# Kernel tuning notes

Measured on AMD Instinct MI355X. Metric: run time of the kernel, lower is better.

The kernel has to match this reference:

```python
import jax, jax.numpy as jnp
import numpy as np

D_MODEL = 1024
N_HEADS = 16
D_K = 64
CHUNK_LEN = 64
B, CHUNKS, NEIGHBORS, NEIGHBOR_LEN = 8, 32, 2, 128
SEQ = CHUNKS * CHUNK_LEN  # 2048
LN_EPS = 1e-5


def setup_inputs() -> dict:
    key = jax.random.key(0)
    ks = jax.random.split(key, 8)
    s = 0.02
    return {
        "h": jax.random.normal(ks[0], (B, SEQ, D_MODEL), dtype=jnp.float32),
        "e": jax.random.normal(ks[1], (B, CHUNKS, NEIGHBORS, NEIGHBOR_LEN, D_MODEL), dtype=jnp.float32),
        "Wq": jax.random.normal(ks[2], (D_MODEL, N_HEADS * D_K), dtype=jnp.float32) * s,
        "bq": jnp.zeros((N_HEADS * D_K,), dtype=jnp.float32),
        "Wk": jax.random.normal(ks[3], (D_MODEL, N_HEADS * D_K), dtype=jnp.float32) * s,
        "bk": jnp.zeros((N_HEADS * D_K,), dtype=jnp.float32),
        "Wv": jax.random.normal(ks[4], (D_MODEL, N_HEADS * D_K), dtype=jnp.float32) * s,
        "bv": jnp.zeros((N_HEADS * D_K,), dtype=jnp.float32),
        "gamma": jnp.ones((D_MODEL,), dtype=jnp.float32),
        "beta": jnp.zeros((D_MODEL,), dtype=jnp.float32),
        "Wo": jax.random.normal(ks[5], (N_HEADS * D_K, D_MODEL), dtype=jnp.float32) * s,
        "bo": jnp.zeros((D_MODEL,), dtype=jnp.float32),
    }


def _layer_norm(x, gamma, beta):
    mu = jnp.mean(x, axis=-1, keepdims=True)
    var = jnp.mean(jnp.square(x - mu), axis=-1, keepdims=True)
    return (x - mu) * jax.lax.rsqrt(var + LN_EPS) * gamma + beta


def reference(h, e, Wq, bq, Wk, bk, Wv, bv, gamma, beta, Wo, bo):
    batch, chunks, neighbors, neighbor_len, d_model = e.shape
    seq = h.shape[1]
    scale = 1.0 / np.sqrt(D_K)
    h_res = h

    # shift so each chunk attends only to completed retrieval chunks
    x = h[:, CHUNK_LEN - 1:]                      # [b, seq-(cl-1), d]
    x = _layer_norm(x, gamma, beta)
    pad = chunks * CHUNK_LEN - x.shape[1]
    x = jnp.pad(x, ((0, 0), (0, pad), (0, 0)))    # [b, chunks*cl, d]
    x = x.reshape(batch, chunks, CHUNK_LEN, d_model)

    q = (x @ Wq + bq).reshape(batch, chunks, CHUNK_LEN, N_HEADS, D_K)
    k = (e @ Wk + bk).reshape(batch, chunks, neighbors, neighbor_len, N_HEADS, D_K)
    v = (e @ Wv + bv).reshape(batch, chunks, neighbors, neighbor_len, N_HEADS, D_K)

    attn = jnp.einsum('bcihd,bcnjhd->bchinj', q, k) * scale   # [b,c,h,i,n,j]
    a_shape = attn.shape
    attn = jax.nn.softmax(attn.reshape(*a_shape[:4], -1), axis=-1).reshape(a_shape)

    o = jnp.einsum('bchinj,bcnjhd->bcihd', attn, v)           # [b,c,i,h,d]
    o = o.reshape(batch, chunks * CHUNK_LEN, N_HEADS * D_K)
    o = o @ Wo + bo
    # undo the shift: left-pad by chunk_len-1, truncate to seq
    o = jnp.pad(o, ((0, 0), (CHUNK_LEN - 1, 0), (0, 0)))[:, :seq]
    return o + h_res
```

## Files before the change

kernel.cpp:

```cpp
#include <hip/hip_runtime.h>
#include <hip/hip_bf16.h>

typedef __attribute__((ext_vector_type(8))) short bf16x8;
typedef __attribute__((ext_vector_type(4))) float f32x4;
typedef __attribute__((ext_vector_type(8))) unsigned short u16x8;

static __device__ __forceinline__ unsigned short f2bf(float f) {
  unsigned int u = __builtin_bit_cast(unsigned int, f);
  u += 0x7fffu + ((u >> 16) & 1u);
  return (unsigned short)(u >> 16);
}
static __device__ __forceinline__ unsigned int pk2(float lo, float hi) {
  return (unsigned int)f2bf(lo) | ((unsigned int)f2bf(hi) << 16);
}
static __device__ __forceinline__ void gload_lds16(const void* g, void* l) {
  __builtin_amdgcn_global_load_lds(
      (__attribute__((address_space(1))) void*)(g),
      (__attribute__((address_space(3))) void*)(l), 16, 0, 0);
}

__global__ __launch_bounds__(256) void cvt_bf16(const float* __restrict__ in,
                                                unsigned short* __restrict__ out,
                                                long n8) {
  const long stride = (long)gridDim.x * 256;
  for (long i = (long)blockIdx.x * 256 + threadIdx.x; i < n8; i += stride) {
    const float4 a = ((const float4*)in)[2 * i];
    const float4 b = ((const float4*)in)[2 * i + 1];
    uint4 w;
    w.x = pk2(a.x, a.y);
    w.y = pk2(a.z, a.w);
    w.z = pk2(b.x, b.y);
    w.w = pk2(b.z, b.w);
    ((uint4*)out)[i] = w;
  }
}

__global__ __launch_bounds__(256) void transpose_w(const float* __restrict__ W,
                                                   unsigned short* __restrict__ WT) {
  __shared__ float tile[64][65];
  const int bx = blockIdx.x;
  const int by = blockIdx.y;
  const int t = threadIdx.x;
  const int rr = t >> 6;
  const int cc = t & 63;
#pragma unroll
  for (int i = 0; i < 16; ++i) {
    int r = i * 4 + rr;
    tile[r][cc] = W[(size_t)(by * 64 + r) * 1024 + bx * 64 + cc];
  }
  __syncthreads();
#pragma unroll
  for (int i = 0; i < 16; ++i) {
    int n = i * 4 + rr;
    WT[(size_t)(bx * 64 + n) * 1024 + by * 64 + cc] = f2bf(tile[cc][n]);
  }
}

__global__ __launch_bounds__(256) void ln_kernel(const float* __restrict__ H,
                                                 const float* __restrict__ gamma,
                                                 const float* __restrict__ beta,
                                                 unsigned short* __restrict__ X) {
  const int row = blockIdx.x;
  const int b = row >> 11;
  const int t = row & 2047;
  const int tid = threadIdx.x;
  uint2* xo = (uint2*)(X + (size_t)row * 1024);
  if (t >= 1985) {
    uint2 z;
    z.x = 0;
    z.y = 0;
    xo[tid] = z;
    return;
  }
  const float4* hp = (const float4*)(H + (size_t)(b * 2048 + t + 63) * 1024);
  float4 v = hp[tid];
  float s = v.x + v.y + v.z + v.w;
  float q = v.x * v.x + v.y * v.y + v.z * v.z + v.w * v.w;
#pragma unroll
  for (int off = 32; off > 0; off >>= 1) {
    s += __shfl_down(s, off);
    q += __shfl_down(q, off);
  }
  __shared__ float red[8];
  const int lane = tid & 63, wid = tid >> 6;
  if (lane == 0) {
    red[wid] = s;
    red[4 + wid] = q;
  }
  __syncthreads();
  s = red[0] + red[1] + red[2] + red[3];
  q = red[4] + red[5] + red[6] + red[7];
  const float mu = s * (1.0f / 1024.0f);
  const float var = q * (1.0f / 1024.0f) - mu * mu;
  const float rs = rsqrtf(var + 1e-5f);
  const float4 g = ((const float4*)gamma)[tid];
  const float4 bb = ((const float4*)beta)[tid];
  uint2 w;
  w.x = pk2((v.x - mu) * rs * g.x + bb.x, (v.y - mu) * rs * g.y + bb.y);
  w.y = pk2((v.z - mu) * rs * g.z + bb.z, (v.w - mu) * rs * g.w + bb.w);
  xo[tid] = w;
}

__global__ __launch_bounds__(256) void fill_head(const float* __restrict__ H,
                                                 float* __restrict__ OUT) {
  const int idx = blockIdx.x * 256 + threadIdx.x;
  const int b = idx / 16128;
  const int rem = idx - b * 16128;
  const size_t off = (size_t)b * 524288 + rem;
  ((float4*)OUT)[off] = ((const float4*)H)[off];
}

#define FENCE_BAR()                                  \
  {                                                  \
    asm volatile("" ::: "memory");                   \
    __builtin_amdgcn_s_barrier();                    \
    __builtin_amdgcn_sched_barrier(0);               \
  }
#define VMW2() asm volatile("s_waitcnt vmcnt(2)" ::: "memory")

#define LDA_(mh, buf)                                                                   \
  {                                                                                     \
    const char* base_ = (const char*)&lds[buf][wm][0];                                  \
    _Pragma("unroll") for (int mi = 0; mi < 4; ++mi) {                                  \
      const int r_ = (mh) * 64 + mi * 16 + lrow;                                        \
      af[mi][0] = *(const bf16x8*)(base_ + r_ * 128 + (((0 + lk) ^ (r_ & 7)) * 16));    \
      af[mi][1] = *(const bf16x8*)(base_ + r_ * 128 + (((4 + lk) ^ (r_ & 7)) * 16));    \
    }                                                                                   \
  }
#define LDB_(nh, buf)                                                                   \
  {                                                                                     \
    const char* base_ = (const char*)&lds[buf][2 + (wn >> 1)][0];                       \
    _Pragma("unroll") for (int ni = 0; ni < 2; ++ni) {                                  \
      const int r_ = (wn & 1) * 64 + (nh) * 32 + ni * 16 + lrow;                        \
      bfr[nh][ni][0] =                                                                  \
          *(const bf16x8*)(base_ + r_ * 128 + (((0 + lk) ^ (r_ & 7)) * 16));            \
      bfr[nh][ni][1] =                                                                  \
          *(const bf16x8*)(base_ + r_ * 128 + (((4 + lk) ^ (r_ & 7)) * 16));            \
    }                                                                                   \
  }
#define MMA_(mh, nh)                                                                    \
  {                                                                                     \
    __builtin_amdgcn_s_setprio(1);                                                      \
    _Pragma("unroll") for (int mi = 0; mi < 4; ++mi)                                    \
        _Pragma("unroll") for (int ni = 0; ni < 2; ++ni) {                              \
      acc[(mh) * 4 + mi][(nh) * 2 + ni] = __builtin_amdgcn_mfma_f32_16x16x32_bf16(      \
          af[mi][0], bfr[nh][ni][0], acc[(mh) * 4 + mi][(nh) * 2 + ni], 0, 0, 0);       \
      acc[(mh) * 4 + mi][(nh) * 2 + ni] = __builtin_amdgcn_mfma_f32_16x16x32_bf16(      \
          af[mi][1], bfr[nh][ni][1], acc[(mh) * 4 + mi][(nh) * 2 + ni], 0, 0, 0);       \
    }                                                                                   \
    __builtin_amdgcn_s_setprio(0);                                                      \
  }

template <int MODE>
__global__ __launch_bounds__(512, 2) void gemm256(
    const unsigned short* __restrict__ A, const unsigned short* __restrict__ BT,
    const float* __restrict__ bias1, const float* __restrict__ bias2,
    unsigned short* __restrict__ C1, unsigned short* __restrict__ C2,
    const float* __restrict__ H, float* __restrict__ OUT) {
  __shared__ alignas(16) unsigned short lds[2][4][128 * 64];
  const int tid = threadIdx.x;
  const int lane = tid & 63;
  const int wid = tid >> 6;
  const int wm = wid >> 2, wn = wid & 3;
  const int lrow = lane & 15, lk = lane >> 4;

  const int nx = gridDim.x;
  const int orig = blockIdx.y * nx + blockIdx.x;
  const int cpx = (nx * gridDim.y) >> 3;
  const int swz = (orig & 7) * cpx + (orig >> 3);
  const int m0 = (swz / nx) * 256;
  const int n0 = (swz % nx) * 256;

  f32x4 acc[8][4] = {};
  bf16x8 af[4][2], bfr[2][2][2];

  auto STAGE = [&](int slot, int kt) {
    const int buf = kt & 1;
    const int kc = kt < 16 ? kt : 15;
    const unsigned short* src = (slot < 2) ? A + (size_t)(m0 + slot * 128) * 1024
                                           : BT + (size_t)(n0 + (slot - 2) * 128) * 1024;
    unsigned short* dst = &lds[buf][slot][0];
#pragma unroll
    for (int l = 0; l < 2; ++l) {
      const int row = l * 64 + wid * 8 + (lane >> 3);
      const int ch = (lane & 7) ^ (row & 7);
      gload_lds16(src + (size_t)row * 1024 + kc * 64 + ch * 8,
                  (char*)dst + (l * 64 + wid * 8) * 128);
    }
  };

  STAGE(0, 0);
  STAGE(1, 0);
  STAGE(2, 0);
  STAGE(3, 0);
  STAGE(0, 1);
  VMW2();
  __builtin_amdgcn_s_barrier();

  for (int it = 0; it < 8; ++it) {
    const int t = 2 * it;
    LDA_(0, 0);
    LDB_(0, 0);
    STAGE(1, t + 1);
    FENCE_BAR();
    MMA_(0, 0);
    FENCE_BAR();
    LDB_(1, 0);
    STAGE(2, t + 1);
    FENCE_BAR();
    MMA_(0, 1);
    FENCE_BAR();
    LDA_(1, 0);
    STAGE(3, t + 1);
    FENCE_BAR();
    MMA_(1, 1);
    FENCE_BAR();
    STAGE(0, t + 2);
    FENCE_BAR();
    MMA_(1, 0);
    VMW2();
    FENCE_BAR();
    LDA_(0, 1);
    LDB_(0, 1);
    STAGE(1, t + 2);
    FENCE_BAR();
    MMA_(0, 0);
    FENCE_BAR();
    LDB_(1, 1);
    STAGE(2, t + 2);
    FENCE_BAR();
    MMA_(0, 1);
    FENCE_BAR();
    LDA_(1, 1);
    STAGE(3, t + 2);
    FENCE_BAR();
    MMA_(1, 1);
    FENCE_BAR();
    STAGE(0, t + 3);
    FENCE_BAR();
    MMA_(1, 0);
    VMW2();
    FENCE_BAR();
  }

  if (MODE == 0) {
    const float* bsel = (n0 < 1024) ? bias1 : bias2;
    const int cbase = (n0 < 1024) ? n0 : (n0 - 1024);
    unsigned short* Cp0 = (n0 < 1024) ? C1 : C2;
    float bsv[4];
#pragma unroll
    for (int N = 0; N < 4; ++N) bsv[N] = bsel[cbase + wn * 64 + N * 16 + lrow];
    float* arr = (float*)&lds[0][0][0];
    const int q4 = lane >> 4;
    __syncthreads();
#pragma unroll
    for (int p = 0; p < 4; ++p) {
      if (wm == (p >> 1)) {
#pragma unroll
        for (int mb = 0; mb < 4; ++mb) {
          const int M = (p & 1) * 4 + mb;
#pragma unroll
          for (int N = 0; N < 4; ++N) {
            const int cl = wn * 64 + N * 16 + lrow;
#pragma unroll
            for (int r = 0; r < 4; ++r) {
              arr[(mb * 16 + q4 * 4 + r) * 260 + cl] = acc[M][N][r] + bsv[N];
            }
          }
        }
      }
      __syncthreads();
#pragma unroll
      for (int k = 0; k < 4; ++k) {
        const int chunk = k * 512 + tid;
        const int row = chunk >> 5;
        const int c8 = chunk & 31;
        const float* s = arr + row * 260 + c8 * 8;
        float4 f0 = *(const float4*)(s);
        float4 f1 = *(const float4*)(s + 4);
        uint4 w;
        w.x = pk2(f0.x, f0.y);
        w.y = pk2(f0.z, f0.w);
        w.z = pk2(f1.x, f1.y);
        w.w = pk2(f1.z, f1.w);
        *(uint4*)(Cp0 + (size_t)(m0 + p * 64 + row) * 1024 + cbase + c8 * 8) = w;
      }
      __syncthreads();
    }
  } else {
    const int r0 = lane >> 4;
#pragma unroll
    for (int N = 0; N < 4; ++N) {
      const int col = n0 + wn * 64 + N * 16 + lrow;
      const float bsv = bias1[col];
#pragma unroll
      for (int M = 0; M < 8; ++M) {
        const int row = m0 + wm * 128 + M * 16 + r0 * 4;
#pragma unroll
        for (int r = 0; r < 4; ++r) {
          const int gr = row + r;
          if ((gr & 2047) < 1985) {
            const size_t idx = (size_t)(gr + 63) * 1024 + col;
            OUT[idx] = H[idx] + acc[M][N][r] + bsv;
          }
        }
      }
    }
  }
}

__global__ __launch_bounds__(256) void attn_kernel(
    const unsigned short* __restrict__ Q, const unsigned short* __restrict__ K,
    const unsigned short* __restrict__ V, unsigned short* __restrict__ O) {
  __shared__ alignas(16) unsigned short k_lds[256 * 64];
  __shared__ alignas(16) unsigned short v_t[64 * 256];
  const int w = ((blockIdx.x & 7) << 9) | (blockIdx.x >> 3);
  const int h = w & 15;
  const int bc = w >> 4;
  const int tid = threadIdx.x;
  const int lane = tid & 63;
  const int wid = tid >> 6;
  const size_t kv0 = (size_t)bc * 256 * 1024 + h * 64;

  bf16x8 qf[2];
  {
    const size_t qrow = (size_t)bc * 64 + wid * 16 + (lane & 15);
    const unsigned short* qp = Q + qrow * 1024 + h * 64 + (lane >> 4) * 8;
    qf[0] = *(const bf16x8*)(qp);
    qf[1] = *(const bf16x8*)(qp + 32);
  }
#pragma unroll
  for (int it = 0; it < 8; ++it) {
    const int j = it * 32 + (tid >> 3);
    const int c = tid & 7;
    const uint4 kv = *(const uint4*)(K + kv0 + (size_t)j * 1024 + c * 8);
    *(uint4*)((char*)k_lds + j * 128 + ((c ^ (j & 7)) * 16)) = kv;
  }
  {
    const int j = (tid >> 1) * 2;
    const int half = tid & 1;
#pragma unroll
    for (int cc2 = 0; cc2 < 4; ++cc2) {
      const int chunk = half * 4 + cc2;
      const int d0 = chunk * 8;
      u16x8 a = *(const u16x8*)(V + kv0 + (size_t)j * 1024 + d0);
      u16x8 b = *(const u16x8*)(V + kv0 + (size_t)(j + 1) * 1024 + d0);
#pragma unroll
      for (int dd = 0; dd < 8; ++dd) {
        const int d = d0 + dd;
        unsigned int p = (unsigned int)a[dd] | ((unsigned int)b[dd] << 16);
        *(unsigned int*)((char*)v_t + d * 512 + (((j >> 3) ^ (d & 7)) * 16) + ((j & 7) * 2)) = p;
      }
    }
  }
  __syncthreads();

  f32x4 accs[16] = {};
#pragma unroll
  for (int jt = 0; jt < 16; ++jt) {
#pragma unroll
    for (int ks = 0; ks < 2; ++ks) {
      const int r = jt * 16 + (lane & 15);
      bf16x8 kf = *(const bf16x8*)((const char*)k_lds + r * 128 +
                                   (((ks * 4 + (lane >> 4)) ^ (r & 7)) * 16));
      accs[jt] = __builtin_amdgcn_mfma_f32_16x16x32_bf16(qf[ks], kf, accs[jt], 0, 0, 0);
    }
  }
  __syncthreads();

  float inv_[4];
#pragma unroll
  for (int r = 0; r < 4; ++r) {
    float m = accs[0][r];
#pragma unroll
    for (int jt = 1; jt < 16; ++jt) m = fmaxf(m, accs[jt][r]);
#pragma unroll
    for (int mk = 1; mk < 16; mk <<= 1) m = fmaxf(m, __shfl_xor(m, mk));
    float s = 0.f;
#pragma unroll
    for (int jt = 0; jt < 16; ++jt) {
      float p = __expf((accs[jt][r] - m) * 0.125f);
      accs[jt][r] = p;
      s += p;
    }
#pragma unroll
    for (int mk = 1; mk < 16; mk <<= 1) s += __shfl_xor(s, mk);
    inv_[r] = 1.0f / s;
  }
  char* pbase = (char*)k_lds + wid * 8192;
  {
    const int jc = lane & 15;
    const int i0 = (lane >> 4) * 4;
#pragma unroll
    for (int jt = 0; jt < 16; ++jt) {
      const int j = jt * 16 + jc;
#pragma unroll
      for (int r = 0; r < 4; ++r) {
        const int i = i0 + r;
        *(unsigned short*)(pbase + i * 512 + (((j >> 3) ^ (i & 7)) * 16) + ((j & 7) * 2)) =
            f2bf(accs[jt][r] * inv_[r]);
      }
    }
  }
  __syncthreads();

  f32x4 acco[4] = {};
#pragma unroll
  for (int jb = 0; jb < 8; ++jb) {
    const int i = lane & 15;
    bf16x8 pf = *(const bf16x8*)(pbase + i * 512 + (((jb * 4 + (lane >> 4)) ^ (i & 7)) * 16));
#pragma unroll
    for (int ni = 0; ni < 4; ++ni) {
      const int d = ni * 16 + (lane & 15);
      bf16x8 vf = *(const bf16x8*)((const char*)v_t + d * 512 +
                                   (((jb * 4 + (lane >> 4)) ^ (d & 7)) * 16));
      acco[ni] = __builtin_amdgcn_mfma_f32_16x16x32_bf16(pf, vf, acco[ni], 0, 0, 0);
    }
  }
  {
    const size_t row0 = (size_t)bc * 64 + wid * 16 + (lane >> 4) * 4;
#pragma unroll
    for (int ni = 0; ni < 4; ++ni) {
      const int col = h * 64 + ni * 16 + (lane & 15);
#pragma unroll
      for (int r = 0; r < 4; ++r) {
        O[(row0 + r) * 1024 + col] = f2bf(acco[ni][r]);
      }
    }
  }
}

extern "C" void kernel_launch(void* const* d_in, const int* in_sizes, int n_in,
                              void* d_out, int out_size, void* d_ws, size_t ws_size,
                              hipStream_t stream) {
  const float* h = (const float*)d_in[0];
  const float* e = (const float*)d_in[1];
  const float* Wq = (const float*)d_in[2];
  const float* bq = (const float*)d_in[3];
  const float* Wk = (const float*)d_in[4];
  const float* bk = (const float*)d_in[5];
  const float* Wv = (const float*)d_in[6];
  const float* bv = (const float*)d_in[7];
  const float* gamma = (const float*)d_in[8];
  const float* beta = (const float*)d_in[9];
  const float* Wo = (const float*)d_in[10];
  const float* bo = (const float*)d_in[11];
  float* out = (float*)d_out;

  char* ws = (char*)d_ws;
  unsigned short* x = (unsigned short*)ws;
  unsigned short* q = (unsigned short*)(ws + (32ull << 20));
  unsigned short* kbuf = (unsigned short*)(ws + (64ull << 20));
  unsigned short* vbuf = (unsigned short*)(ws + (192ull << 20));
  unsigned short* ebf = (unsigned short*)(ws + (320ull << 20));
  unsigned short* wqT = (unsigned short*)(ws + (448ull << 20));
  unsigned short* wkvT = (unsigned short*)(ws + (450ull << 20));
  unsigned short* woT = (unsigned short*)(ws + (454ull << 20));
  unsigned short* o = x;

  dim3 tb(256);
  cvt_bf16<<<2048, tb, 0, stream>>>(e, ebf, 8388608L);
  transpose_w<<<dim3(16, 16), tb, 0, stream>>>(Wq, wqT);
  transpose_w<<<dim3(16, 16), tb, 0, stream>>>(Wk, wkvT);
  transpose_w<<<dim3(16, 16), tb, 0, stream>>>(Wv, wkvT + 1024 * 1024);
  transpose_w<<<dim3(16, 16), tb, 0, stream>>>(Wo, woT);
  ln_kernel<<<16384, tb, 0, stream>>>(h, gamma, beta, x);
  gemm256<0><<<dim3(4, 64), dim3(512), 0, stream>>>(x, wqT, bq, nullptr, q, nullptr,
                                                    nullptr, nullptr);
  gemm256<0><<<dim3(8, 256), dim3(512), 0, stream>>>(ebf, wkvT, bk, bv, kbuf, vbuf,
                                                     nullptr, nullptr);
  attn_kernel<<<4096, tb, 0, stream>>>(q, kbuf, vbuf, o);
  fill_head<<<504, tb, 0, stream>>>(h, out);
  gemm256<1><<<dim3(4, 64), dim3(512), 0, stream>>>(o, woT, bo, nullptr, nullptr, nullptr,
                                                    h, out);
}
```

Measured before the change: 569.4 us.

## Double-buffer A fragments and cut barriers in the GEMM main loop

The 256x256 bf16 GEMM main loop gets separate register sets for the two A halves and two B halves. The second A and B fragments are now loaded while the first MMA block is still pending, and about half of the block-wide barriers are replaced by scheduling-only fences. This is meant to lower barrier stall time and overlap LDS reads with MFMA work. The cost is more VGPR pressure under the 512-thread, 2-block launch bound, plus reliance on the remaining barriers to keep LDS buffer reuse safe.

```diff
diff --git a/kernel.cpp b/kernel.cpp
--- a/kernel.cpp
+++ b/kernel.cpp
@@ -110,43 +110,42 @@
   ((float4*)OUT)[off] = ((const float4*)H)[off];
 }
 
-#define FENCE_BAR()                                  \
-  {                                                  \
-    asm volatile("" ::: "memory");                   \
-    __builtin_amdgcn_s_barrier();                    \
-    __builtin_amdgcn_sched_barrier(0);               \
-  }
+#define BAR()                                 \
+  {                                           \
+    asm volatile("" ::: "memory");            \
+    __builtin_amdgcn_s_barrier();             \
+    __builtin_amdgcn_sched_barrier(0);        \
+  }
+#define SB0() __builtin_amdgcn_sched_barrier(0)
 #define VMW2() asm volatile("s_waitcnt vmcnt(2)" ::: "memory")
 
-#define LDA_(mh, buf)                                                                   \
+#define LDA_(dst, mh, buf)                                                              \
   {                                                                                     \
     const char* base_ = (const char*)&lds[buf][wm][0];                                  \
     _Pragma("unroll") for (int mi = 0; mi < 4; ++mi) {                                  \
       const int r_ = (mh) * 64 + mi * 16 + lrow;                                        \
-      af[mi][0] = *(const bf16x8*)(base_ + r_ * 128 + (((0 + lk) ^ (r_ & 7)) * 16));    \
-      af[mi][1] = *(const bf16x8*)(base_ + r_ * 128 + (((4 + lk) ^ (r_ & 7)) * 16));    \
+      dst[mi][0] = *(const bf16x8*)(base_ + r_ * 128 + (((0 + lk) ^ (r_ & 7)) * 16));   \
+      dst[mi][1] = *(const bf16x8*)(base_ + r_ * 128 + (((4 + lk) ^ (r_ & 7)) * 16));   \
     }                                                                                   \
   }
-#define LDB_(nh, buf)                                                                   \
+#define LDB_(dst, nh, buf)                                                              \
   {                                                                                     \
     const char* base_ = (const char*)&lds[buf][2 + (wn >> 1)][0];                       \
     _Pragma("unroll") for (int ni = 0; ni < 2; ++ni) {                                  \
       const int r_ = (wn & 1) * 64 + (nh) * 32 + ni * 16 + lrow;                        \
-      bfr[nh][ni][0] =                                                                  \
-          *(const bf16x8*)(base_ + r_ * 128 + (((0 + lk) ^ (r_ & 7)) * 16));            \
-      bfr[nh][ni][1] =                                                                  \
-          *(const bf16x8*)(base_ + r_ * 128 + (((4 + lk) ^ (r_ & 7)) * 16));            \
+      dst[ni][0] = *(const bf16x8*)(base_ + r_ * 128 + (((0 + lk) ^ (r_ & 7)) * 16));   \
+      dst[ni][1] = *(const bf16x8*)(base_ + r_ * 128 + (((4 + lk) ^ (r_ & 7)) * 16));   \
     }                                                                                   \
   }
-#define MMA_(mh, nh)                                                                    \
+#define MMA_(mh, nh, A, B)                                                              \
   {                                                                                     \
     __builtin_amdgcn_s_setprio(1);                                                      \
     _Pragma("unroll") for (int mi = 0; mi < 4; ++mi)                                    \
         _Pragma("unroll") for (int ni = 0; ni < 2; ++ni) {                              \
       acc[(mh) * 4 + mi][(nh) * 2 + ni] = __builtin_amdgcn_mfma_f32_16x16x32_bf16(      \
-          af[mi][0], bfr[nh][ni][0], acc[(mh) * 4 + mi][(nh) * 2 + ni], 0, 0, 0);       \
+          A[mi][0], B[ni][0], acc[(mh) * 4 + mi][(nh) * 2 + ni], 0, 0, 0);              \
       acc[(mh) * 4 + mi][(nh) * 2 + ni] = __builtin_amdgcn_mfma_f32_16x16x32_bf16(      \
-          af[mi][1], bfr[nh][ni][1], acc[(mh) * 4 + mi][(nh) * 2 + ni], 0, 0, 0);       \
+          A[mi][1], B[ni][1], acc[(mh) * 4 + mi][(nh) * 2 + ni], 0, 0, 0);              \
     }                                                                                   \
     __builtin_amdgcn_s_setprio(0);                                                      \
   }
@@ -172,7 +171,7 @@
   const int n0 = (swz % nx) * 256;
 
   f32x4 acc[8][4] = {};
-  bf16x8 af[4][2], bfr[2][2][2];
+  bf16x8 af[4][2], ax[4][2], b0[2][2], b1[2][2];
 
   auto STAGE = [&](int slot, int kt) {
     const int buf = kt & 1;
@@ -199,48 +198,42 @@
 
   for (int it = 0; it < 8; ++it) {
     const int t = 2 * it;
-    LDA_(0, 0);
-    LDB_(0, 0);
+    LDA_(af, 0, 0);
+    LDB_(b0, 0, 0);
     STAGE(1, t + 1);
-    FENCE_BAR();
-    MMA_(0, 0);
-    FENCE_BAR();
-    LDB_(1, 0);
+    MMA_(0, 0, af, b0);
+    SB0();
+    LDB_(b1, 1, 0);
+    LDA_(ax, 1, 0);
+    BAR();
     STAGE(2, t + 1);
-    FENCE_BAR();
-    MMA_(0, 1);
-    FENCE_BAR();
-    LDA_(1, 0);
+    MMA_(0, 1, af, b1);
+    BAR();
     STAGE(3, t + 1);
-    FENCE_BAR();
-    MMA_(1, 1);
-    FENCE_BAR();
+    MMA_(1, 1, ax, b1);
+    BAR();
     STAGE(0, t + 2);
-    FENCE_BAR();
-    MMA_(1, 0);
+    MMA_(1, 0, ax, b0);
     VMW2();
-    FENCE_BAR();
-    LDA_(0, 1);
-    LDB_(0, 1);
+    BAR();
+    LDA_(af, 0, 1);
+    LDB_(b0, 0, 1);
     STAGE(1, t + 2);
-    FENCE_BAR();
-    MMA_(0, 0);
-    FENCE_BAR();
-    LDB_(1, 1);
+    MMA_(0, 0, af, b0);
+    SB0();
+    LDB_(b1, 1, 1);
+    LDA_(ax, 1, 1);
+    BAR();
     STAGE(2, t + 2);
-    FENCE_BAR();
-    MMA_(0, 1);
-    FENCE_BAR();
-    LDA_(1, 1);
+    MMA_(0, 1, af, b1);
+    BAR();
     STAGE(3, t + 2);
-    FENCE_BAR();
-    MMA_(1, 1);
-    FENCE_BAR();
+    MMA_(1, 1, ax, b1);
+    BAR();
     STAGE(0, t + 3);
-    FENCE_BAR();
-    MMA_(1, 0);
+    MMA_(1, 0, ax, b0);
     VMW2();
-    FENCE_BAR();
+    BAR();
   }
 
   if (MODE == 0) {
```

Measured after the change: 623.1 us. 1.09x slower.
